# Optimization experiments

Hardware: AMD Instinct MI355X
Metric: run time of the kernel (lower is better)

Reference implementation:

```python
import jax, jax.numpy as jnp
import numpy as np

N = 262144          # number of tracks (batched Python loop)
E = 256             # QD similarity embedding dim
MOTION_DIMS = 7     # observed 3D box dims
STATE_DIMS = 10     # motion_dims + 3 location velocities
MOMENTUM = 0.8      # memory_momentum
INIT_POS_VAR = 10.0     # kf3d_init_mean_cov position variance
INIT_VEL_VAR = 10000.0  # kf3d_init_mean_cov velocity variance


def _kf_mats():
    # constant-velocity transition: x,y,z += vx,vy,vz
    F = jnp.eye(STATE_DIMS, dtype=jnp.float32)
    F = F.at[jnp.arange(3), MOTION_DIMS + jnp.arange(3)].set(1.0)
    Q = jnp.eye(STATE_DIMS, dtype=jnp.float32)      # cov_motion_q
    R = jnp.eye(MOTION_DIMS, dtype=jnp.float32)     # cov_project_r
    return F, Q, R


def setup_inputs() -> dict:
    key = jax.random.key(0)
    ks = jax.random.split(key, 12)
    A = 0.1 * jax.random.normal(ks[4], (N, STATE_DIMS, STATE_DIMS), dtype=jnp.float32)
    prev_covs = jnp.einsum('nij,nkj->nik', A, A) + jnp.eye(STATE_DIMS, dtype=jnp.float32)
    return {
        'boxes_3d': jax.random.normal(ks[0], (N, 12), dtype=jnp.float32),
        'obs_boxes_3d': jax.random.normal(ks[1], (N, MOTION_DIMS), dtype=jnp.float32),
        'prev_boxes7': jax.random.normal(ks[2], (N, MOTION_DIMS), dtype=jnp.float32),
        'prev_means': jax.random.normal(ks[3], (N, STATE_DIMS), dtype=jnp.float32),
        'prev_covs': prev_covs,
        'prev_velocities': jax.random.normal(ks[5], (N, MOTION_DIMS), dtype=jnp.float32),
        'prev_embeddings': jax.random.normal(ks[6], (N, E), dtype=jnp.float32),
        'embeddings': jax.random.normal(ks[7], (N, E), dtype=jnp.float32),
        'acc_frames': jax.random.randint(ks[8], (N,), 0, 10, dtype=jnp.int32),
        'frame_gap': jax.random.randint(ks[9], (N,), 0, 5, dtype=jnp.int32) + 1,
        'matched': jax.random.randint(ks[10], (N,), 0, 2).astype(bool),
        'fps': 2,
    }


def reference(boxes_3d, obs_boxes_3d, prev_boxes7, prev_means, prev_covs,
              prev_velocities, prev_embeddings, embeddings,
              acc_frames, frame_gap, matched, fps):
    F, Q, R = _kf_mats()
    m1 = matched[:, None]

    # ---- matched branch: kf3d_update (H = eye(7,10), so H P H^T = P[:7,:7]) ----
    PHt = prev_covs[:, :, :MOTION_DIMS]                        # P H^T  [N,10,7]
    S = prev_covs[:, :MOTION_DIMS, :MOTION_DIMS] + R           # [N,7,7]
    Kt = jnp.linalg.solve(S, jnp.swapaxes(PHt, 1, 2))          # S^-1 H P  [N,7,10]
    K = jnp.swapaxes(Kt, 1, 2)                                 # [N,10,7]
    innov = obs_boxes_3d - prev_means[:, :MOTION_DIMS]
    mean_u = prev_means + jnp.einsum('nij,nj->ni', K, innov)   # [N,10]
    cov_u = prev_covs - jnp.einsum('nij,njk,nlk->nil', K, S, K)

    # ---- predict location after update (only loc is consumed) ----
    pred_loc = jnp.einsum('ij,nj->ni', F, mean_u)[:, :3]

    # ---- unmatched branch: kf3d_init_mean_cov ----
    mean_i = jnp.concatenate(
        [obs_boxes_3d, jnp.zeros((obs_boxes_3d.shape[0], 3), dtype=obs_boxes_3d.dtype)], axis=1)
    diag_i = jnp.concatenate([jnp.full((MOTION_DIMS,), INIT_POS_VAR, jnp.float32),
                              jnp.full((3,), INIT_VEL_VAR, jnp.float32)])
    cov_i = jnp.diag(diag_i)                                   # [10,10], broadcast in where

    new_means = jnp.where(m1, mean_u, mean_i)
    new_covs = jnp.where(matched[:, None, None], cov_u, cov_i[None])

    # ---- boxes_3d scatter write (matched rows) ----
    pd = mean_u[:, :MOTION_DIMS]
    b_upd = jnp.concatenate(
        [pd[:, :6],                               # cols 0..5
         boxes_3d[:, 6:8],                        # cols 6,7 untouched
         pd[:, 6:7],                              # col 8 = yaw
         (pred_loc - mean_u[:, :3]) * fps],       # cols 9..11 velocity
        axis=1)
    new_boxes_3d = jnp.where(m1, b_upd, boxes_3d)

    # ---- velocity running average ----
    gap = frame_gap.astype(jnp.float32)[:, None]
    acc = acc_frames.astype(jnp.float32)
    vel_obs = (pd - prev_boxes7) / gap
    vel_m = (prev_velocities * acc[:, None] + vel_obs) / (acc[:, None] + 1.0)
    new_velocities = jnp.where(m1, vel_m, jnp.zeros_like(vel_m))
    new_acc_frames = jnp.where(matched, acc + 1.0, jnp.zeros_like(acc))

    # ---- embedding EMA ----
    emb_m = (1.0 - MOMENTUM) * prev_embeddings + MOMENTUM * embeddings
    new_embeddings = jnp.where(m1, emb_m, embeddings)

    return (new_boxes_3d, new_means, new_covs, new_velocities, new_embeddings, new_acc_frames)
```

## Files before the change

kernel.cpp:

```cpp
#include <hip/hip_runtime.h>

#define MD 7
#define SD 10

__global__ void detect_kernel(const unsigned char* __restrict__ mbytes,
                              int nbytes, int* __restrict__ flag)
{
    if (blockIdx.x == 0 && threadIdx.x == 0) {
        int f = 0;
        for (int i = 0; i < nbytes; i++) {
            if ((i & 3) != 0 && mbytes[i] != 0) { f = 1; break; }
        }
        *flag = f;
    }
}

__device__ __forceinline__ bool get_matched(const void* mptr, int n, int flag)
{
    if (flag) return ((const unsigned char*)mptr)[n] != 0;
    return ((const int*)mptr)[n] != 0;
}

__device__ __forceinline__ float load_scalar_f(const int* p)
{
    int v = *p;
    if (v >= -1000000 && v <= 1000000) return (float)v;
    union { int i; float f; } u; u.i = v; return u.f;
}

__global__ __launch_bounds__(256) void kf_kernel(
    const float* __restrict__ boxes,
    const float* __restrict__ obs,
    const float* __restrict__ pb7,
    const float* __restrict__ pmean,
    const float* __restrict__ pcov,
    const float* __restrict__ pvel,
    const int*   __restrict__ accf,
    const int*   __restrict__ fgap,
    const void*  __restrict__ matched,
    const int*   __restrict__ fps_p,
    const int*   __restrict__ mflag,
    float* __restrict__ oboxes,
    float* __restrict__ omean,
    float* __restrict__ ocov,
    float* __restrict__ ovel,
    float* __restrict__ oacc,
    int N)
{
    int n = blockIdx.x * blockDim.x + threadIdx.x;
    if (n >= N) return;

    const int  flag = *mflag;
    const bool m    = get_matched(matched, n, flag);
    const float fps = load_scalar_f(fps_p);

    float bx[12];
    {
        const float4* bp = (const float4*)(boxes + (size_t)n * 12);
        float4 a = bp[0], b = bp[1], c = bp[2];
        bx[0]=a.x; bx[1]=a.y; bx[2]=a.z;  bx[3]=a.w;
        bx[4]=b.x; bx[5]=b.y; bx[6]=b.z;  bx[7]=b.w;
        bx[8]=c.x; bx[9]=c.y; bx[10]=c.z; bx[11]=c.w;
    }
    float ob[7];
#pragma unroll
    for (int j = 0; j < 7; j++) ob[j] = obs[(size_t)n * 7 + j];

    float nb[12], nmu[10], CV[100], nvel[7], nacc;

    if (m) {
        const float4* cp = (const float4*)(pcov + (size_t)n * 100);
#pragma unroll
        for (int i = 0; i < 25; i++) {
            float4 v = cp[i];
            CV[4*i+0] = v.x; CV[4*i+1] = v.y; CV[4*i+2] = v.z; CV[4*i+3] = v.w;
        }
        float mu[10];
        {
            const float2* mp = (const float2*)(pmean + (size_t)n * 10);
#pragma unroll
            for (int i = 0; i < 5; i++) { float2 v = mp[i]; mu[2*i] = v.x; mu[2*i+1] = v.y; }
        }

        float L[7][7];
#pragma unroll
        for (int k = 0; k < 7; k++) {
            float d = CV[k*10 + k] + 1.0f;
#pragma unroll
            for (int q = 0; q < k; q++) d -= L[k][q] * L[k][q];
            float dk = sqrtf(d);
            L[k][k] = dk;
            float inv = 1.0f / dk;
#pragma unroll
            for (int i = k + 1; i < 7; i++) {
                float s = CV[i*10 + k];
#pragma unroll
                for (int q = 0; q < k; q++) s -= L[i][q] * L[k][q];
                L[i][k] = s * inv;
            }
        }

        float X[7][10];
#pragma unroll
        for (int j = 0; j < 7; j++) {
            float rinv = 1.0f / L[j][j];
#pragma unroll
            for (int l = 0; l < 10; l++) {
                float s = CV[l*10 + j];
#pragma unroll
                for (int q = 0; q < j; q++) s -= L[j][q] * X[q][l];
                X[j][l] = s * rinv;
            }
        }
#pragma unroll
        for (int j = 6; j >= 0; j--) {
            float rinv = 1.0f / L[j][j];
#pragma unroll
            for (int l = 0; l < 10; l++) {
                float s = X[j][l];
#pragma unroll
                for (int q = j + 1; q < 7; q++) s -= L[q][j] * X[q][l];
                X[j][l] = s * rinv;
            }
        }

        float innov[7];
#pragma unroll
        for (int j = 0; j < 7; j++) innov[j] = ob[j] - mu[j];
        float mu_u[10];
#pragma unroll
        for (int l = 0; l < 10; l++) {
            float s = mu[l];
#pragma unroll
            for (int j = 0; j < 7; j++) s += X[j][l] * innov[j];
            mu_u[l] = s;
        }

#pragma unroll
        for (int l = 0; l < 10; l++) {
            float r[10];
#pragma unroll
            for (int c = 0; c < 10; c++) {
                float s = 0.0f;
#pragma unroll
                for (int j = 0; j < 7; j++) s += CV[l*10 + j] * X[j][c];
                r[c] = CV[l*10 + c] - s;
            }
#pragma unroll
            for (int c = 0; c < 10; c++) CV[l*10 + c] = r[c];
        }

        nb[0] = mu_u[0]; nb[1] = mu_u[1]; nb[2] = mu_u[2];
        nb[3] = mu_u[3]; nb[4] = mu_u[4]; nb[5] = mu_u[5];
        nb[6] = bx[6];   nb[7] = bx[7];   nb[8] = mu_u[6];
        nb[9]  = mu_u[7] * fps;
        nb[10] = mu_u[8] * fps;
        nb[11] = mu_u[9] * fps;

        float gap = (float)fgap[n];
        float acc = (float)accf[n];
#pragma unroll
        for (int j = 0; j < 7; j++) {
            float vobs = (mu_u[j] - pb7[(size_t)n*7 + j]) / gap;
            nvel[j] = (pvel[(size_t)n*7 + j] * acc + vobs) / (acc + 1.0f);
        }
        nacc = acc + 1.0f;
#pragma unroll
        for (int l = 0; l < 10; l++) nmu[l] = mu_u[l];
    } else {
#pragma unroll
        for (int i = 0; i < 100; i++) CV[i] = 0.0f;
#pragma unroll
        for (int l = 0; l < 7; l++)  CV[l*11] = 10.0f;
#pragma unroll
        for (int l = 7; l < 10; l++) CV[l*11] = 10000.0f;
#pragma unroll
        for (int j = 0; j < 7; j++) nmu[j] = ob[j];
        nmu[7] = nmu[8] = nmu[9] = 0.0f;
#pragma unroll
        for (int i = 0; i < 12; i++) nb[i] = bx[i];
#pragma unroll
        for (int j = 0; j < 7; j++) nvel[j] = 0.0f;
        nacc = 0.0f;
    }

    {
        float4* op = (float4*)(oboxes + (size_t)n * 12);
        op[0] = make_float4(nb[0], nb[1], nb[2],  nb[3]);
        op[1] = make_float4(nb[4], nb[5], nb[6],  nb[7]);
        op[2] = make_float4(nb[8], nb[9], nb[10], nb[11]);
    }
    {
        float2* op = (float2*)(omean + (size_t)n * 10);
#pragma unroll
        for (int i = 0; i < 5; i++) op[i] = make_float2(nmu[2*i], nmu[2*i+1]);
    }
    {
        float4* op = (float4*)(ocov + (size_t)n * 100);
#pragma unroll
        for (int i = 0; i < 25; i++)
            op[i] = make_float4(CV[4*i], CV[4*i+1], CV[4*i+2], CV[4*i+3]);
    }
#pragma unroll
    for (int j = 0; j < 7; j++) ovel[(size_t)n*7 + j] = nvel[j];
    oacc[n] = nacc;
}

__global__ __launch_bounds__(256) void emb_kernel(
    const float* __restrict__ pemb,
    const float* __restrict__ emb,
    const void*  __restrict__ matched,
    const int*   __restrict__ mflag,
    float* __restrict__ oemb,
    int N)
{
    int gid  = blockIdx.x * 256 + threadIdx.x;
    int row  = gid >> 6;
    if (row >= N) return;
    int lane = gid & 63;

    const bool m = get_matched(matched, row, *mflag);
    size_t idx = (size_t)row * 64 + lane;

    float4 e = ((const float4*)emb)[idx];
    float4 o;
    if (m) {
        float4 p = ((const float4*)pemb)[idx];
        o.x = 0.2f * p.x + 0.8f * e.x;
        o.y = 0.2f * p.y + 0.8f * e.y;
        o.z = 0.2f * p.z + 0.8f * e.z;
        o.w = 0.2f * p.w + 0.8f * e.w;
    } else {
        o = e;
    }
    ((float4*)oemb)[idx] = o;
}

extern "C" void kernel_launch(void* const* d_in, const int* in_sizes, int n_in,
                              void* d_out, int out_size, void* d_ws, size_t ws_size,
                              hipStream_t stream)
{
    const float* boxes  = (const float*)d_in[0];
    const float* obs    = (const float*)d_in[1];
    const float* pb7    = (const float*)d_in[2];
    const float* pmean  = (const float*)d_in[3];
    const float* pcov   = (const float*)d_in[4];
    const float* pvel   = (const float*)d_in[5];
    const float* pemb   = (const float*)d_in[6];
    const float* emb    = (const float*)d_in[7];
    const int*   accf   = (const int*)d_in[8];
    const int*   fgap   = (const int*)d_in[9];
    const void*  matched= d_in[10];
    const int*   fps_p  = (const int*)d_in[11];
    const int N = in_sizes[8];

    float* out = (float*)d_out;
    float* oboxes = out;
    float* omean  = out + (size_t)N * 12;
    float* ocov   = out + (size_t)N * 22;
    float* ovel   = out + (size_t)N * 122;
    float* oemb   = out + (size_t)N * 129;
    float* oacc   = out + (size_t)N * 385;

    int* mflag = (int*)d_ws;

    detect_kernel<<<1, 64, 0, stream>>>((const unsigned char*)matched, 1024, mflag);
    kf_kernel<<<(N + 255) / 256, 256, 0, stream>>>(
        boxes, obs, pb7, pmean, pcov, pvel, accf, fgap, matched, fps_p, mflag,
        oboxes, omean, ocov, ovel, oacc, N);
    emb_kernel<<<N / 4, 256, 0, stream>>>(pemb, emb, matched, mflag, oemb, N);
}
```

Before: 892.8 us.

## Cut KF kernel register pressure and parallelize matched-dtype detection

The Kalman update now keeps only the needed covariance blocks (10x7 columns plus the 3x3 velocity block) in registers. It uses symmetry to rebuild the upper-right block and writes results straight to global memory inside each branch, instead of holding a full 100-float matrix and staging output arrays. The unmatched branch streams boxes through and writes constant covariance directly, and a few divides become reciprocal multiplies. The single-thread dtype detection becomes a 64-thread ballot, and launch bounds ask for 2 blocks per SIMD. The goal is lower VGPR use and spills for higher occupancy; reading the upper-right covariance block from its transpose assumes the input covariance is symmetric.

```diff
diff --git a/kernel.cpp b/kernel.cpp
--- a/kernel.cpp
+++ b/kernel.cpp
@@ -1,18 +1,14 @@
 #include <hip/hip_runtime.h>
-
-#define MD 7
-#define SD 10
 
 __global__ void detect_kernel(const unsigned char* __restrict__ mbytes,
                               int nbytes, int* __restrict__ flag)
 {
-    if (blockIdx.x == 0 && threadIdx.x == 0) {
-        int f = 0;
-        for (int i = 0; i < nbytes; i++) {
-            if ((i & 3) != 0 && mbytes[i] != 0) { f = 1; break; }
-        }
-        *flag = f;
-    }
+    int t = threadIdx.x;
+    int f = 0;
+    for (int i = t; i < nbytes; i += 64)
+        if ((i & 3) != 0 && mbytes[i] != 0) f = 1;
+    unsigned long long b = __ballot(f != 0);
+    if (t == 0) *flag = (b != 0ULL) ? 1 : 0;
 }
 
 __device__ __forceinline__ bool get_matched(const void* mptr, int n, int flag)
@@ -28,7 +24,7 @@
     union { int i; float f; } u; u.i = v; return u.f;
 }
 
-__global__ __launch_bounds__(256) void kf_kernel(
+__global__ __launch_bounds__(256, 2) void kf_kernel(
     const float* __restrict__ boxes,
     const float* __restrict__ obs,
     const float* __restrict__ pb7,
@@ -52,28 +48,28 @@
 
     const int  flag = *mflag;
     const bool m    = get_matched(matched, n, flag);
-    const float fps = load_scalar_f(fps_p);
-
-    float bx[12];
-    {
-        const float4* bp = (const float4*)(boxes + (size_t)n * 12);
-        float4 a = bp[0], b = bp[1], c = bp[2];
-        bx[0]=a.x; bx[1]=a.y; bx[2]=a.z;  bx[3]=a.w;
-        bx[4]=b.x; bx[5]=b.y; bx[6]=b.z;  bx[7]=b.w;
-        bx[8]=c.x; bx[9]=c.y; bx[10]=c.z; bx[11]=c.w;
-    }
+
     float ob[7];
 #pragma unroll
     for (int j = 0; j < 7; j++) ob[j] = obs[(size_t)n * 7 + j];
 
-    float nb[12], nmu[10], CV[100], nvel[7], nacc;
-
     if (m) {
-        const float4* cp = (const float4*)(pcov + (size_t)n * 100);
-#pragma unroll
-        for (int i = 0; i < 25; i++) {
-            float4 v = cp[i];
-            CV[4*i+0] = v.x; CV[4*i+1] = v.y; CV[4*i+2] = v.z; CV[4*i+3] = v.w;
+        const float fps = load_scalar_f(fps_p);
+
+        float W[10][7], V3[3][3];
+        {
+            const float4* cp = (const float4*)(pcov + (size_t)n * 100);
+#pragma unroll
+            for (int i = 0; i < 25; i++) {
+                float4 v = cp[i];
+                float vv[4] = {v.x, v.y, v.z, v.w};
+#pragma unroll
+                for (int k = 0; k < 4; k++) {
+                    const int e = 4 * i + k, l = e / 10, c = e % 10;
+                    if (c < 7)            W[l][c]        = vv[k];
+                    else if (l >= 7)      V3[l-7][c-7]   = vv[k];
+                }
+            }
         }
         float mu[10];
         {
@@ -85,7 +81,7 @@
         float L[7][7];
 #pragma unroll
         for (int k = 0; k < 7; k++) {
-            float d = CV[k*10 + k] + 1.0f;
+            float d = W[k][k] + 1.0f;
 #pragma unroll
             for (int q = 0; q < k; q++) d -= L[k][q] * L[k][q];
             float dk = sqrtf(d);
@@ -93,7 +89,7 @@
             float inv = 1.0f / dk;
 #pragma unroll
             for (int i = k + 1; i < 7; i++) {
-                float s = CV[i*10 + k];
+                float s = W[i][k];
 #pragma unroll
                 for (int q = 0; q < k; q++) s -= L[i][q] * L[k][q];
                 L[i][k] = s * inv;
@@ -106,7 +102,7 @@
             float rinv = 1.0f / L[j][j];
 #pragma unroll
             for (int l = 0; l < 10; l++) {
-                float s = CV[l*10 + j];
+                float s = W[l][j];
 #pragma unroll
                 for (int q = 0; q < j; q++) s -= L[j][q] * X[q][l];
                 X[j][l] = s * rinv;
@@ -136,74 +132,84 @@
             mu_u[l] = s;
         }
 
-#pragma unroll
-        for (int l = 0; l < 10; l++) {
-            float r[10];
-#pragma unroll
-            for (int c = 0; c < 10; c++) {
-                float s = 0.0f;
-#pragma unroll
-                for (int j = 0; j < 7; j++) s += CV[l*10 + j] * X[j][c];
-                r[c] = CV[l*10 + c] - s;
-            }
-#pragma unroll
-            for (int c = 0; c < 10; c++) CV[l*10 + c] = r[c];
-        }
-
-        nb[0] = mu_u[0]; nb[1] = mu_u[1]; nb[2] = mu_u[2];
-        nb[3] = mu_u[3]; nb[4] = mu_u[4]; nb[5] = mu_u[5];
-        nb[6] = bx[6];   nb[7] = bx[7];   nb[8] = mu_u[6];
-        nb[9]  = mu_u[7] * fps;
-        nb[10] = mu_u[8] * fps;
-        nb[11] = mu_u[9] * fps;
-
-        float gap = (float)fgap[n];
-        float acc = (float)accf[n];
+        {
+            float4* op = (float4*)(ocov + (size_t)n * 100);
+#pragma unroll
+            for (int i = 0; i < 25; i++) {
+                float r[4];
+#pragma unroll
+                for (int k = 0; k < 4; k++) {
+                    const int e = 4 * i + k, l = e / 10, c = e % 10;
+                    float base = (c < 7) ? W[l][c]
+                               : ((l < 7) ? W[c][l] : V3[l-7][c-7]);
+                    float s = 0.0f;
+#pragma unroll
+                    for (int j = 0; j < 7; j++) s += W[l][j] * X[j][c];
+                    r[k] = base - s;
+                }
+                op[i] = make_float4(r[0], r[1], r[2], r[3]);
+            }
+        }
+
+        float bx6, bx7;
+        {
+            const float4* bp = (const float4*)(boxes + (size_t)n * 12);
+            float4 b = bp[1];
+            bx6 = b.z; bx7 = b.w;
+        }
+        {
+            float4* op = (float4*)(oboxes + (size_t)n * 12);
+            op[0] = make_float4(mu_u[0], mu_u[1], mu_u[2], mu_u[3]);
+            op[1] = make_float4(mu_u[4], mu_u[5], bx6,     bx7);
+            op[2] = make_float4(mu_u[6], mu_u[7] * fps, mu_u[8] * fps, mu_u[9] * fps);
+        }
+        {
+            float2* op = (float2*)(omean + (size_t)n * 10);
+#pragma unroll
+            for (int i = 0; i < 5; i++) op[i] = make_float2(mu_u[2*i], mu_u[2*i+1]);
+        }
+
+        float gap  = (float)fgap[n];
+        float acc  = (float)accf[n];
+        float ginv = 1.0f / gap;
+        float ainv = 1.0f / (acc + 1.0f);
 #pragma unroll
         for (int j = 0; j < 7; j++) {
-            float vobs = (mu_u[j] - pb7[(size_t)n*7 + j]) / gap;
-            nvel[j] = (pvel[(size_t)n*7 + j] * acc + vobs) / (acc + 1.0f);
-        }
-        nacc = acc + 1.0f;
-#pragma unroll
-        for (int l = 0; l < 10; l++) nmu[l] = mu_u[l];
+            float vobs = (mu_u[j] - pb7[(size_t)n*7 + j]) * ginv;
+            ovel[(size_t)n*7 + j] = (pvel[(size_t)n*7 + j] * acc + vobs) * ainv;
+        }
+        oacc[n] = acc + 1.0f;
     } else {
-#pragma unroll
-        for (int i = 0; i < 100; i++) CV[i] = 0.0f;
-#pragma unroll
-        for (int l = 0; l < 7; l++)  CV[l*11] = 10.0f;
-#pragma unroll
-        for (int l = 7; l < 10; l++) CV[l*11] = 10000.0f;
-#pragma unroll
-        for (int j = 0; j < 7; j++) nmu[j] = ob[j];
-        nmu[7] = nmu[8] = nmu[9] = 0.0f;
-#pragma unroll
-        for (int i = 0; i < 12; i++) nb[i] = bx[i];
-#pragma unroll
-        for (int j = 0; j < 7; j++) nvel[j] = 0.0f;
-        nacc = 0.0f;
+        {
+            const float4* bp = (const float4*)(boxes + (size_t)n * 12);
+            float4* op = (float4*)(oboxes + (size_t)n * 12);
+            op[0] = bp[0]; op[1] = bp[1]; op[2] = bp[2];
+        }
+        {
+            float2* op = (float2*)(omean + (size_t)n * 10);
+            op[0] = make_float2(ob[0], ob[1]);
+            op[1] = make_float2(ob[2], ob[3]);
+            op[2] = make_float2(ob[4], ob[5]);
+            op[3] = make_float2(ob[6], 0.0f);
+            op[4] = make_float2(0.0f, 0.0f);
+        }
+        {
+            float4* op = (float4*)(ocov + (size_t)n * 100);
+#pragma unroll
+            for (int i = 0; i < 25; i++) {
+                float r[4];
+#pragma unroll
+                for (int k = 0; k < 4; k++) {
+                    const int e = 4 * i + k, l = e / 10, c = e % 10;
+                    r[k] = (l == c) ? ((l < 7) ? 10.0f : 10000.0f) : 0.0f;
+                }
+                op[i] = make_float4(r[0], r[1], r[2], r[3]);
+            }
+        }
+#pragma unroll
+        for (int j = 0; j < 7; j++) ovel[(size_t)n*7 + j] = 0.0f;
+        oacc[n] = 0.0f;
     }
-
-    {
-        float4* op = (float4*)(oboxes + (size_t)n * 12);
-        op[0] = make_float4(nb[0], nb[1], nb[2],  nb[3]);
-        op[1] = make_float4(nb[4], nb[5], nb[6],  nb[7]);
-        op[2] = make_float4(nb[8], nb[9], nb[10], nb[11]);
-    }
-    {
-        float2* op = (float2*)(omean + (size_t)n * 10);
-#pragma unroll
-        for (int i = 0; i < 5; i++) op[i] = make_float2(nmu[2*i], nmu[2*i+1]);
-    }
-    {
-        float4* op = (float4*)(ocov + (size_t)n * 100);
-#pragma unroll
-        for (int i = 0; i < 25; i++)
-            op[i] = make_float4(CV[4*i], CV[4*i+1], CV[4*i+2], CV[4*i+3]);
-    }
-#pragma unroll
-    for (int j = 0; j < 7; j++) ovel[(size_t)n*7 + j] = nvel[j];
-    oacc[n] = nacc;
 }
 
 __global__ __launch_bounds__(256) void emb_kernel(
@@ -268,5 +274,5 @@
     kf_kernel<<<(N + 255) / 256, 256, 0, stream>>>(
         boxes, obs, pb7, pmean, pcov, pvel, accf, fgap, matched, fps_p, mflag,
         oboxes, omean, ocov, ovel, oacc, N);
-    emb_kernel<<<N / 4, 256, 0, stream>>>(pemb, emb, matched, mflag, oemb, N);
-}
+    emb_kernel<<<(N + 3) / 4, 256, 0, stream>>>(pemb, emb, matched, mflag, oemb, N);
+}
```

New measurement: 852.8 us. 1.05x faster.
